# Kernel tuning notes

Measured on AMD Instinct MI355X. Metric: run time of the kernel, lower is better.

The kernel has to match this reference:

```python
import jax, jax.numpy as jnp
import numpy as np
import math

B, S, D, H = 2, 2048, 1024, 16
DH = D // H  # dim_per_head = 64


def setup_inputs() -> dict:
    key = jax.random.key(0)
    ks = jax.random.split(key, 12)
    s = 1.0 / math.sqrt(D)
    return {
        "key": jax.random.normal(ks[0], (B, S, D), jnp.float32),
        "value": jax.random.normal(ks[1], (B, S, D), jnp.float32),
        "query": jax.random.normal(ks[2], (B, S, D), jnp.float32),
        "mask": jax.random.randint(ks[3], (B, S, S), 0, 2).astype(bool),
        "Wq": jax.random.normal(ks[4], (D, D), jnp.float32) * s,
        "bq": jnp.zeros((D,), jnp.float32),
        "Wk": jax.random.normal(ks[5], (D, D), jnp.float32) * s,
        "bk": jnp.zeros((D,), jnp.float32),
        "Wv": jax.random.normal(ks[6], (D, D), jnp.float32) * s,
        "bv": jnp.zeros((D,), jnp.float32),
        "Wo": jax.random.normal(ks[7], (D, D), jnp.float32) * s,
        "bo": jnp.zeros((D,), jnp.float32),
    }


def _shape(x):
    # [B, S, D] -> [B, H, S, DH]
    return x.reshape(B, -1, H, DH).transpose(0, 2, 1, 3)


def reference(key, value, query, mask, Wq, bq, Wk, bk, Wv, bv, Wo, bo):
    q = _shape(query @ Wq.T + bq)  # [B,H,Sq,DH]
    k = _shape(key @ Wk.T + bk)    # [B,H,Sk,DH]
    v = _shape(value @ Wv.T + bv)  # [B,H,Sk,DH]
    q = q / jnp.sqrt(jnp.asarray(DH, q.dtype))
    scores = jnp.einsum("bhqd,bhkd->bhqk", q, k)
    scores = jnp.where(mask[:, None, :, :], jnp.asarray(-1e18, scores.dtype), scores)
    attn = jax.nn.softmax(scores, axis=-1)
    # dropout is identity in eval/deterministic reference
    ctx = jnp.einsum("bhqk,bhkd->bhqd", attn, v)
    ctx = ctx.transpose(0, 2, 1, 3).reshape(B, -1, D)  # unshape
    return ctx @ Wo.T + bo
```

## Files before the change

### kernel.cpp

```cpp
#include <hip/hip_runtime.h>
#include <math.h>


constexpr int Bc  = 2;
constexpr int Sc  = 2048;
constexpr int Dc  = 1024;
constexpr int Hc  = 16;
constexpr int DHc = 64;
constexpr int BSc = Bc * Sc;

constexpr float LOG2E = 1.4426950408889634f;

typedef __bf16 bf16x8 __attribute__((ext_vector_type(8)));
typedef __bf16 bf16x4 __attribute__((ext_vector_type(4)));
typedef __bf16 bf16x2 __attribute__((ext_vector_type(2)));
typedef float  f32x4  __attribute__((ext_vector_type(4)));
typedef float  f32x16 __attribute__((ext_vector_type(16)));
typedef unsigned uint32x2 __attribute__((ext_vector_type(2)));
typedef unsigned uint32x4 __attribute__((ext_vector_type(4)));

#define GLDS16(gp, lp) __builtin_amdgcn_global_load_lds( \
    (const __attribute__((address_space(1))) void*)(gp), \
    (__attribute__((address_space(3))) void*)(lp), 16, 0, 0)

__global__ __launch_bounds__(256)
void wsplit(const float* __restrict__ W0, const float* __restrict__ W1,
            const float* __restrict__ W2, const float* __restrict__ W3,
            __bf16* __restrict__ out)
{
    const float* src[4] = {W0, W1, W2, W3};
    const int z = blockIdx.y;
    const size_t idx = ((size_t)blockIdx.x * 256 + threadIdx.x) * 4;
    const float4 v = *(const float4*)&src[z][idx];
    bf16x4 o;
    o[0] = (__bf16)v.x; o[1] = (__bf16)v.y; o[2] = (__bf16)v.z; o[3] = (__bf16)v.w;
    *(bf16x4*)&out[(size_t)z * Dc * Dc + idx] = o;
}

__global__ __launch_bounds__(256)
void acast(const float* __restrict__ A0, const float* __restrict__ A1,
           const float* __restrict__ A2, __bf16* __restrict__ out)
{
    const float* src[3] = {A0, A1, A2};
    const int z = blockIdx.y;
    const size_t idx = ((size_t)blockIdx.x * 256 + threadIdx.x) * 8;
    const float4 a = *(const float4*)&src[z][idx];
    const float4 b = *(const float4*)&src[z][idx + 4];
    bf16x8 o;
    o[0] = (__bf16)a.x; o[1] = (__bf16)a.y; o[2] = (__bf16)a.z; o[3] = (__bf16)a.w;
    o[4] = (__bf16)b.x; o[5] = (__bf16)b.y; o[6] = (__bf16)b.z; o[7] = (__bf16)b.w;
    *(bf16x8*)&out[(size_t)z * BSc * Dc + idx] = o;
}

template<int KD>
__device__ __forceinline__ void sweep128bb(const __bf16* __restrict__ A,
                                           const __bf16* __restrict__ Wh,
                                           char* AsB, char* WsB,
                                           int gm0, int gn0, f32x4 acc[4][4])
{
    const int tid  = threadIdx.x;
    const int w    = tid >> 6;
    const int lane = tid & 63;
    const int cc   = lane & 15;
    const int g    = lane >> 4;
    const int wm   = (w & 1) * 64;
    const int wn   = (w >> 1) * 64;

    int wrow[4], wchk[4];
#pragma unroll
    for (int r = 0; r < 4; ++r) {
        const int L = r * 256 + tid;
        wrow[r] = L >> 3;
        wchk[r] = (L & 7) ^ (wrow[r] & 7);
    }

#pragma unroll
    for (int r = 0; r < 4; ++r) {
        GLDS16(Wh + (size_t)(gn0 + wrow[r]) * KD + wchk[r] * 8,
               WsB + (r * 256 + tid) * 16);
        GLDS16(A + (size_t)(gm0 + wrow[r]) * KD + wchk[r] * 8,
               AsB + (r * 256 + tid) * 16);
    }

    for (int it = 0; it < KD / 64; ++it) {
        const char* As = AsB + (it & 1) * 16384;
        const char* Ws = WsB + (it & 1) * 16384;
        __syncthreads();

        if (it + 1 < KD / 64) {
            const int kn = (it + 1) * 64;
            char* Wn = WsB + ((it + 1) & 1) * 16384;
            char* An = AsB + ((it + 1) & 1) * 16384;
#pragma unroll
            for (int r = 0; r < 4; ++r) {
                GLDS16(Wh + (size_t)(gn0 + wrow[r]) * KD + kn + wchk[r] * 8,
                       Wn + (r * 256 + tid) * 16);
                GLDS16(A + (size_t)(gm0 + wrow[r]) * KD + kn + wchk[r] * 8,
                       An + (r * 256 + tid) * 16);
            }
        }

        __builtin_amdgcn_s_setprio(1);
#pragma unroll
        for (int kk = 0; kk < 2; ++kk) {
            const int cb4 = (kk * 4 + g) << 4;
            bf16x8 af[4], bfr[4];
#pragma unroll
            for (int mt = 0; mt < 4; ++mt) {
                const int row = wm + mt * 16 + cc;
                af[mt] = *(const bf16x8*)(As + row * 128 + (cb4 ^ ((row & 7) << 4)));
            }
#pragma unroll
            for (int nt = 0; nt < 4; ++nt) {
                const int row = wn + nt * 16 + cc;
                bfr[nt] = *(const bf16x8*)(Ws + row * 128 + (cb4 ^ ((row & 7) << 4)));
            }
#pragma unroll
            for (int mt = 0; mt < 4; ++mt)
#pragma unroll
                for (int nt = 0; nt < 4; ++nt)
                    acc[mt][nt] = __builtin_amdgcn_mfma_f32_16x16x32_bf16(
                        af[mt], bfr[nt], acc[mt][nt], 0, 0, 0);
        }
        __builtin_amdgcn_s_setprio(0);
    }
}

__device__ __forceinline__ void sweep64p(const __bf16* __restrict__ Ahi,
                                         const __bf16* __restrict__ Alo,
                                         const __bf16* __restrict__ Wh,
                                         char* WsB, char* AhB, char* AlB,
                                         int gm0, int gn0, f32x4 acc[2][4])
{
    const int tid  = threadIdx.x;
    const int w    = tid >> 6;
    const int lane = tid & 63;
    const int cc   = lane & 15;
    const int g    = lane >> 4;
    const int wm   = (w & 1) * 32;
    const int wn   = (w >> 1) * 64;

    int wrow[4], wchk[4];
#pragma unroll
    for (int r = 0; r < 4; ++r) {
        const int L = r * 256 + tid;
        wrow[r] = L >> 3;
        wchk[r] = (L & 7) ^ (wrow[r] & 7);
    }
    int arow[2], achk[2];
#pragma unroll
    for (int r = 0; r < 2; ++r) {
        const int L = r * 256 + tid;
        arow[r] = L >> 3;
        achk[r] = (L & 7) ^ (arow[r] & 7);
    }

#pragma unroll
    for (int r = 0; r < 4; ++r)
        GLDS16(Wh + (size_t)(gn0 + wrow[r]) * Dc + wchk[r] * 8,
               WsB + (r * 256 + tid) * 16);
#pragma unroll
    for (int r = 0; r < 2; ++r) {
        GLDS16(Ahi + (size_t)(gm0 + arow[r]) * Dc + achk[r] * 8,
               AhB + (r * 256 + tid) * 16);
        GLDS16(Alo + (size_t)(gm0 + arow[r]) * Dc + achk[r] * 8,
               AlB + (r * 256 + tid) * 16);
    }

    for (int it = 0; it < Dc / 64; ++it) {
        const char* Ws = WsB + (it & 1) * 16384;
        const char* Ah = AhB + (it & 1) * 8192;
        const char* Al = AlB + (it & 1) * 8192;
        __syncthreads();

        if (it + 1 < Dc / 64) {
            const int kn = (it + 1) * 64;
            char* Wn = WsB + ((it + 1) & 1) * 16384;
            char* Hn = AhB + ((it + 1) & 1) * 8192;
            char* Ln = AlB + ((it + 1) & 1) * 8192;
#pragma unroll
            for (int r = 0; r < 4; ++r)
                GLDS16(Wh + (size_t)(gn0 + wrow[r]) * Dc + kn + wchk[r] * 8,
                       Wn + (r * 256 + tid) * 16);
#pragma unroll
            for (int r = 0; r < 2; ++r) {
                GLDS16(Ahi + (size_t)(gm0 + arow[r]) * Dc + kn + achk[r] * 8,
                       Hn + (r * 256 + tid) * 16);
                GLDS16(Alo + (size_t)(gm0 + arow[r]) * Dc + kn + achk[r] * 8,
                       Ln + (r * 256 + tid) * 16);
            }
        }

        __builtin_amdgcn_s_setprio(1);
#pragma unroll
        for (int kk = 0; kk < 2; ++kk) {
            const int cb4 = (kk * 4 + g) << 4;
            bf16x8 ahi[2], alo[2], bfr[4];
#pragma unroll
            for (int mt = 0; mt < 2; ++mt) {
                const int row = wm + mt * 16 + cc;
                const int off = row * 128 + (cb4 ^ ((row & 7) << 4));
                ahi[mt] = *(const bf16x8*)(Ah + off);
                alo[mt] = *(const bf16x8*)(Al + off);
            }
#pragma unroll
            for (int nt = 0; nt < 4; ++nt) {
                const int row = wn + nt * 16 + cc;
                bfr[nt] = *(const bf16x8*)(Ws + row * 128 + (cb4 ^ ((row & 7) << 4)));
            }
#pragma unroll
            for (int mt = 0; mt < 2; ++mt)
#pragma unroll
                for (int nt = 0; nt < 4; ++nt) {
                    acc[mt][nt] = __builtin_amdgcn_mfma_f32_16x16x32_bf16(
                        ahi[mt], bfr[nt], acc[mt][nt], 0, 0, 0);
                    acc[mt][nt] = __builtin_amdgcn_mfma_f32_16x16x32_bf16(
                        alo[mt], bfr[nt], acc[mt][nt], 0, 0, 0);
                }
        }
        __builtin_amdgcn_s_setprio(0);
    }
}

__global__ __launch_bounds__(256)
void qkv_mfma(const __bf16* __restrict__ Abf, const __bf16* __restrict__ Whi,
              const float* __restrict__ bq, const float* __restrict__ bk,
              const float* __restrict__ bv,
              __bf16* __restrict__ Qo, __bf16* __restrict__ Ko, __bf16* __restrict__ Vt)
{
    __shared__ __align__(16) char smem[65536];

    const int z = blockIdx.y;
    const float* bias = (z == 0) ? bq : (z == 1) ? bk : bv;
    const float scale = (z == 0) ? 0.125f * LOG2E : 1.0f;
    const __bf16* A   = Abf + (size_t)z * BSc * Dc;
    const __bf16* Wh  = Whi + (size_t)z * Dc * Dc;

    const int lb  = (blockIdx.x & 7) * 32 + (blockIdx.x >> 3);
    const int idx = lb & 31;
    const int gm0 = ((lb >> 5) * 4 + (idx & 3)) * 128;
    const int gn0 = (idx >> 2) * 128;

    f32x4 acc[4][4];
#pragma unroll
    for (int mt = 0; mt < 4; ++mt)
#pragma unroll
        for (int nt = 0; nt < 4; ++nt) acc[mt][nt] = {0.f, 0.f, 0.f, 0.f};

    sweep128bb<Dc>(A, Wh, smem, smem + 32768, gm0, gn0, acc);

    const int tid = threadIdx.x;
    const int w = tid >> 6, lane = tid & 63;
    const int cc = lane & 15, g = lane >> 4;
    const int wm = (w & 1) * 64, wn = (w >> 1) * 64;

    float bias4[4];
#pragma unroll
    for (int nt = 0; nt < 4; ++nt) bias4[nt] = bias[gn0 + wn + nt * 16 + cc];

    if (z == 2) {
#pragma unroll
        for (int mt = 0; mt < 4; ++mt)
#pragma unroll
            for (int nt = 0; nt < 4; ++nt) {
                const int col = gn0 + wn + nt * 16 + cc;
                const int h = col >> 6, dh = col & 63;
                const int row0 = gm0 + wm + mt * 16 + g * 4;
                const int b = row0 >> 11, s0 = row0 & 2047;
                bf16x4 vv;
#pragma unroll
                for (int reg = 0; reg < 4; ++reg)
                    vv[reg] = (__bf16)(acc[mt][nt][reg] + bias4[nt]);
                *(bf16x4*)&Vt[(((size_t)(b * Hc + h)) * DHc + dh) * Sc + s0] = vv;
            }
    } else {
        __bf16* O = (z == 0) ? Qo : Ko;
#pragma unroll
        for (int mt = 0; mt < 4; ++mt)
#pragma unroll
            for (int nt = 0; nt < 4; ++nt) {
                const int col = gn0 + wn + nt * 16 + cc;
                const int h = col >> 6, dh = col & 63;
#pragma unroll
                for (int reg = 0; reg < 4; ++reg) {
                    const int row = gm0 + wm + mt * 16 + g * 4 + reg;
                    const int b = row >> 11, s = row & 2047;
                    O[(((size_t)(b * Hc + h)) * Sc + s) * DHc + dh] =
                        (__bf16)((acc[mt][nt][reg] + bias4[nt]) * scale);
                }
            }
    }
}

__global__ __launch_bounds__(256)
void out_mfma(const __bf16* __restrict__ ctxHi, const __bf16* __restrict__ ctxLo,
              const __bf16* __restrict__ Wohi,
              const float* __restrict__ bo, float* __restrict__ out)
{
    __shared__ __align__(16) char smem[65536];

    const int lb = (blockIdx.x & 7) * 64 + (blockIdx.x >> 3);
    const int gm0 = ((lb >> 6) * 8 + (lb & 7)) * 64;
    const int gn0 = ((lb >> 3) & 7) * 128;

    f32x4 acc[2][4];
#pragma unroll
    for (int mt = 0; mt < 2; ++mt)
#pragma unroll
        for (int nt = 0; nt < 4; ++nt) acc[mt][nt] = {0.f, 0.f, 0.f, 0.f};

    sweep64p(ctxHi, ctxLo, Wohi, smem, smem + 32768, smem + 49152, gm0, gn0, acc);

    const int tid = threadIdx.x;
    const int w = tid >> 6, lane = tid & 63;
    const int cc = lane & 15, g = lane >> 4;
    const int wm = (w & 1) * 32, wn = (w >> 1) * 64;

    float bias4[4];
#pragma unroll
    for (int nt = 0; nt < 4; ++nt) bias4[nt] = bo[gn0 + wn + nt * 16 + cc];

#pragma unroll
    for (int mt = 0; mt < 2; ++mt)
#pragma unroll
        for (int nt = 0; nt < 4; ++nt) {
            const int col = gn0 + wn + nt * 16 + cc;
#pragma unroll
            for (int reg = 0; reg < 4; ++reg) {
                const int row = gm0 + wm + mt * 16 + g * 4 + reg;
                out[(size_t)row * Dc + col] = acc[mt][nt][reg] + bias4[nt];
            }
        }
}

__global__ __launch_bounds__(256)
void mask_pack(const int* __restrict__ mask, unsigned long long* __restrict__ out)
{
    const int lane = threadIdx.x & 63;
    const size_t waveBase = ((size_t)blockIdx.x * 4 + (threadIdx.x >> 6)) * 256;
    unsigned long long b0 = __ballot(mask[waveBase + lane]        != 0);
    unsigned long long b1 = __ballot(mask[waveBase + 64 + lane]   != 0);
    unsigned long long b2 = __ballot(mask[waveBase + 128 + lane]  != 0);
    unsigned long long b3 = __ballot(mask[waveBase + 192 + lane]  != 0);
    if (lane == 0) {
        unsigned long long* dst = out + (waveBase >> 6);
        dst[0] = b0; dst[1] = b1; dst[2] = b2; dst[3] = b3;
    }
}

__global__ __launch_bounds__(256, 2)
void attn_mfma(const __bf16* __restrict__ Q, const __bf16* __restrict__ K,
               const __bf16* __restrict__ Vt,
               const unsigned long long* __restrict__ mp,
               __bf16* __restrict__ ctxHi, __bf16* __restrict__ ctxLo)
{
    __shared__ __align__(16) char smem[32768];

    const int tid  = threadIdx.x;
    const int w    = tid >> 6;
    const int lane = tid & 63;
    const int c    = lane & 31;
    const int u    = lane >> 5;
    const int bh   = blockIdx.y;
    const int b    = bh >> 4;
    const int h    = bh & 15;
    const int qw   = blockIdx.x * 128 + w * 32;

    const __bf16* Qb  = Q  + (size_t)bh * Sc * DHc;
    const __bf16* Kb  = K  + (size_t)bh * Sc * DHc;
    const __bf16* Vtb = Vt + (size_t)bh * DHc * Sc;

    bf16x8 qa[4];
#pragma unroll
    for (int ch = 0; ch < 4; ++ch)
        qa[ch] = *(const bf16x8*)&Qb[(size_t)(qw + c) * DHc + ch * 16 + u * 8];

    f32x16 o[2];
#pragma unroll
    for (int dt = 0; dt < 2; ++dt)
#pragma unroll
        for (int i = 0; i < 16; ++i) o[dt][i] = 0.f;
    float lp[4] = {0.f, 0.f, 0.f, 0.f};

    const int ci[2] = {tid, 256 + tid};
    int rowi[2], ski[2];
#pragma unroll
    for (int i = 0; i < 2; ++i) {
        rowi[i] = ci[i] >> 3;
        ski[i]  = (ci[i] & 7) ^ (rowi[i] & 7);
    }

#pragma unroll
    for (int i = 0; i < 2; ++i) {
        GLDS16(Kb + (size_t)rowi[i] * DHc + ski[i] * 8,
               smem + ci[i] * 16);
        GLDS16(Vtb + (size_t)rowi[i] * Sc + ski[i] * 8,
               smem + 8192 + ci[i] * 16);
    }

    for (int it = 0; it < 32; ++it) {
        const char* Ks = smem + (it & 1) * 16384;
        const char* Vs = Ks + 8192;

        __syncthreads();

        if (it + 1 < 32) {
            char* Kn = smem + ((it + 1) & 1) * 16384;
            const int kn = (it + 1) * 64;
#pragma unroll
            for (int i = 0; i < 2; ++i) {
                GLDS16(Kb + (size_t)(kn + rowi[i]) * DHc + ski[i] * 8,
                       Kn + ci[i] * 16);
                GLDS16(Vtb + (size_t)rowi[i] * Sc + kn + ski[i] * 8,
                       Kn + 8192 + ci[i] * 16);
            }
        }

        const unsigned long long mw =
            mp[((size_t)(b * Sc + qw + c) << 5) + it];

        f32x16 sc[2];
        __builtin_amdgcn_s_setprio(1);
#pragma unroll
        for (int nt = 0; nt < 2; ++nt) {
            f32x16 z;
#pragma unroll
            for (int i = 0; i < 16; ++i) z[i] = -24.f;
#pragma unroll
            for (int ch = 0; ch < 4; ++ch) {
                const int row = nt * 32 + c;
                const bf16x8 kb = *(const bf16x8*)
                    (Ks + row * 128 + ((ch * 32 + u * 16) ^ ((row & 7) << 4)));
                z = __builtin_amdgcn_mfma_f32_32x32x16_bf16(kb, qa[ch], z, 0, 0, 0);
            }
            sc[nt] = z;
        }
        __builtin_amdgcn_s_setprio(0);

        unsigned pk[2][4][2];
#pragma unroll
        for (int nt = 0; nt < 2; ++nt)
#pragma unroll
            for (int rr = 0; rr < 4; ++rr) {
                const unsigned nib =
                    (unsigned)(mw >> (nt * 32 + rr * 8 + u * 4)) & 0xFu;
                float pv[4];
#pragma unroll
                for (int r = 0; r < 4; ++r) {
                    float p = __builtin_amdgcn_exp2f(sc[nt][rr * 4 + r]);
                    p = (nib & (1u << r)) ? 0.f : p;
                    lp[rr] += p;
                    pv[r] = p;
                }
                bf16x2 t0; t0[0] = (__bf16)pv[0]; t0[1] = (__bf16)pv[1];
                bf16x2 t1; t1[0] = (__bf16)pv[2]; t1[1] = (__bf16)pv[3];
                pk[nt][rr][0] = __builtin_bit_cast(unsigned, t0);
                pk[nt][rr][1] = __builtin_bit_cast(unsigned, t1);
            }

        bf16x8 pa[4];
#pragma unroll
        for (int kc = 0; kc < 4; ++kc) {
            const int nt = kc >> 1;
            const int r0 = (kc & 1) * 2;
            uint32x2 s0 = __builtin_amdgcn_permlane32_swap(
                pk[nt][r0][0], pk[nt][r0 + 1][0], false, false);
            uint32x2 s1 = __builtin_amdgcn_permlane32_swap(
                pk[nt][r0][1], pk[nt][r0 + 1][1], false, false);
            uint32x4 wds;
            wds[0] = s0[0]; wds[1] = s1[0]; wds[2] = s0[1]; wds[3] = s1[1];
            pa[kc] = __builtin_bit_cast(bf16x8, wds);
        }

        __builtin_amdgcn_s_setprio(1);
#pragma unroll
        for (int dt = 0; dt < 2; ++dt)
#pragma unroll
            for (int kc = 0; kc < 4; ++kc) {
                const int row = dt * 32 + c;
                const bf16x8 vb = *(const bf16x8*)
                    (Vs + row * 128 + ((kc * 32 + u * 16) ^ ((row & 7) << 4)));
                o[dt] = __builtin_amdgcn_mfma_f32_32x32x16_bf16(pa[kc], vb, o[dt], 0, 0, 0);
            }
        __builtin_amdgcn_s_setprio(0);
    }

    float lsum = (lp[0] + lp[1]) + (lp[2] + lp[3]);
    lsum += __shfl_xor(lsum, 32);
    const float linv = 1.0f / lsum;

    float inv[16];
#pragma unroll
    for (int i = 0; i < 16; ++i)
        inv[i] = __shfl(linv, (i & 3) + 8 * (i >> 2) + 4 * u);

#pragma unroll
    for (int dt = 0; dt < 2; ++dt)
#pragma unroll
        for (int i = 0; i < 16; ++i) {
            const int q = qw + (i & 3) + 8 * (i >> 2) + 4 * u;
            const size_t idx = ((size_t)b * Sc + q) * Dc + h * 64 + dt * 32 + c;
            const float v = o[dt][i] * inv[i];
            const __bf16 hi = (__bf16)v;
            ctxHi[idx] = hi;
            ctxLo[idx] = (__bf16)(v - (float)hi);
        }
}

extern "C" void kernel_launch(void* const* d_in, const int* in_sizes, int n_in,
                              void* d_out, int out_size, void* d_ws, size_t ws_size,
                              hipStream_t stream)
{
    const float* key   = (const float*)d_in[0];
    const float* value = (const float*)d_in[1];
    const float* query = (const float*)d_in[2];
    const int*   mask  = (const int*)  d_in[3];
    const float* Wq    = (const float*)d_in[4];
    const float* bq    = (const float*)d_in[5];
    const float* Wk    = (const float*)d_in[6];
    const float* bk    = (const float*)d_in[7];
    const float* Wv    = (const float*)d_in[8];
    const float* bv    = (const float*)d_in[9];
    const float* Wo    = (const float*)d_in[10];
    const float* bo    = (const float*)d_in[11];
    float* out = (float*)d_out;

    char* wsb = (char*)d_ws;
    __bf16* Qbf  = (__bf16*)(wsb);
    __bf16* Kbf  = (__bf16*)(wsb + ((size_t)8  << 20));
    __bf16* Vt   = (__bf16*)(wsb + ((size_t)16 << 20));
    unsigned long long* mpk = (unsigned long long*)(wsb + ((size_t)32 << 20));
    __bf16* Whi  = (__bf16*)(wsb + ((size_t)33 << 20));
    __bf16* ctxHi = (__bf16*)(wsb + ((size_t)41 << 20));
    __bf16* ctxLo = (__bf16*)(wsb + ((size_t)49 << 20));
    __bf16* Abf  = (__bf16*)(wsb + ((size_t)57 << 20));

    dim3 gws(Dc * Dc / (256 * 4), 4);
    wsplit<<<gws, 256, 0, stream>>>(Wq, Wk, Wv, Wo, Whi);

    dim3 gac(BSc * Dc / (256 * 8), 3);
    acast<<<gac, 256, 0, stream>>>(query, key, value, Abf);

    dim3 gqkv(256, 3);
    qkv_mfma<<<gqkv, 256, 0, stream>>>(Abf, Whi, bq, bk, bv, Qbf, Kbf, Vt);

    const int mask_n = Bc * Sc * Sc;
    mask_pack<<<mask_n / 1024, 256, 0, stream>>>(mask, mpk);

    dim3 gattn(Sc / 128, Bc * Hc);
    attn_mfma<<<gattn, 256, 0, stream>>>(Qbf, Kbf, Vt, mpk, ctxHi, ctxLo);

    out_mfma<<<dim3(512), 256, 0, stream>>>(ctxHi, ctxLo, Whi + (size_t)3 * Dc * Dc,
                                            bo, out);
}
```

Measured before the change: 250.3 us.

## Fuse prep kernels into one launch and stage two KV tiles per barrier

```diff
diff --git a/kernel.cpp b/kernel.cpp
--- a/kernel.cpp
+++ b/kernel.cpp
@@ -24,32 +24,51 @@
     (__attribute__((address_space(3))) void*)(lp), 16, 0, 0)
 
 __global__ __launch_bounds__(256)
-void wsplit(const float* __restrict__ W0, const float* __restrict__ W1,
-            const float* __restrict__ W2, const float* __restrict__ W3,
-            __bf16* __restrict__ out)
-{
-    const float* src[4] = {W0, W1, W2, W3};
-    const int z = blockIdx.y;
-    const size_t idx = ((size_t)blockIdx.x * 256 + threadIdx.x) * 4;
-    const float4 v = *(const float4*)&src[z][idx];
-    bf16x4 o;
-    o[0] = (__bf16)v.x; o[1] = (__bf16)v.y; o[2] = (__bf16)v.z; o[3] = (__bf16)v.w;
-    *(bf16x4*)&out[(size_t)z * Dc * Dc + idx] = o;
-}
-
-__global__ __launch_bounds__(256)
-void acast(const float* __restrict__ A0, const float* __restrict__ A1,
-           const float* __restrict__ A2, __bf16* __restrict__ out)
-{
-    const float* src[3] = {A0, A1, A2};
-    const int z = blockIdx.y;
-    const size_t idx = ((size_t)blockIdx.x * 256 + threadIdx.x) * 8;
-    const float4 a = *(const float4*)&src[z][idx];
-    const float4 b = *(const float4*)&src[z][idx + 4];
-    bf16x8 o;
-    o[0] = (__bf16)a.x; o[1] = (__bf16)a.y; o[2] = (__bf16)a.z; o[3] = (__bf16)a.w;
-    o[4] = (__bf16)b.x; o[5] = (__bf16)b.y; o[6] = (__bf16)b.z; o[7] = (__bf16)b.w;
-    *(bf16x8*)&out[(size_t)z * BSc * Dc + idx] = o;
+void prep(const float* __restrict__ W0, const float* __restrict__ W1,
+          const float* __restrict__ W2, const float* __restrict__ W3,
+          __bf16* __restrict__ Whi,
+          const float* __restrict__ A0, const float* __restrict__ A1,
+          const float* __restrict__ A2, __bf16* __restrict__ Abf,
+          const int* __restrict__ mask, unsigned long long* __restrict__ mpk)
+{
+    const int bid = blockIdx.x;
+    const int tid = threadIdx.x;
+
+    if (bid < 4096) {
+        const float* src[4] = {W0, W1, W2, W3};
+        const int z  = bid >> 10;
+        const int bx = bid & 1023;
+        const size_t idx = ((size_t)bx * 256 + tid) * 4;
+        const float4 v = *(const float4*)&src[z][idx];
+        bf16x4 o;
+        o[0] = (__bf16)v.x; o[1] = (__bf16)v.y;
+        o[2] = (__bf16)v.z; o[3] = (__bf16)v.w;
+        *(bf16x4*)&Whi[(size_t)z * Dc * Dc + idx] = o;
+    } else if (bid < 10240) {
+        const float* src[3] = {A0, A1, A2};
+        const int lin = bid - 4096;
+        const int z  = lin >> 11;
+        const int bx = lin & 2047;
+        const size_t idx = ((size_t)bx * 256 + tid) * 8;
+        const float4 a = *(const float4*)&src[z][idx];
+        const float4 b = *(const float4*)&src[z][idx + 4];
+        bf16x8 o;
+        o[0] = (__bf16)a.x; o[1] = (__bf16)a.y; o[2] = (__bf16)a.z; o[3] = (__bf16)a.w;
+        o[4] = (__bf16)b.x; o[5] = (__bf16)b.y; o[6] = (__bf16)b.z; o[7] = (__bf16)b.w;
+        *(bf16x8*)&Abf[(size_t)z * BSc * Dc + idx] = o;
+    } else {
+        const int bx   = bid - 10240;
+        const int lane = tid & 63;
+        const size_t waveBase = ((size_t)bx * 4 + (tid >> 6)) * 256;
+        unsigned long long b0 = __ballot(mask[waveBase + lane]        != 0);
+        unsigned long long b1 = __ballot(mask[waveBase + 64 + lane]   != 0);
+        unsigned long long b2 = __ballot(mask[waveBase + 128 + lane]  != 0);
+        unsigned long long b3 = __ballot(mask[waveBase + 192 + lane]  != 0);
+        if (lane == 0) {
+            unsigned long long* dst = mpk + (waveBase >> 6);
+            dst[0] = b0; dst[1] = b1; dst[2] = b2; dst[3] = b3;
+        }
+    }
 }
 
 template<int KD>
@@ -333,19 +352,93 @@
         }
 }
 
-__global__ __launch_bounds__(256)
-void mask_pack(const int* __restrict__ mask, unsigned long long* __restrict__ out)
-{
-    const int lane = threadIdx.x & 63;
-    const size_t waveBase = ((size_t)blockIdx.x * 4 + (threadIdx.x >> 6)) * 256;
-    unsigned long long b0 = __ballot(mask[waveBase + lane]        != 0);
-    unsigned long long b1 = __ballot(mask[waveBase + 64 + lane]   != 0);
-    unsigned long long b2 = __ballot(mask[waveBase + 128 + lane]  != 0);
-    unsigned long long b3 = __ballot(mask[waveBase + 192 + lane]  != 0);
-    if (lane == 0) {
-        unsigned long long* dst = out + (waveBase >> 6);
-        dst[0] = b0; dst[1] = b1; dst[2] = b2; dst[3] = b3;
-    }
+__device__ __forceinline__ void stage_pair(const __bf16* Kb, const __bf16* Vtb,
+                                           char* H, int t0,
+                                           int rowi0, int ski0, int ci0,
+                                           int rowi1, int ski1, int ci1)
+{
+#pragma unroll
+    for (int s = 0; s < 2; ++s) {
+        char* B = H + s * 16384;
+        const int kn = (t0 + s) * 64;
+        GLDS16(Kb + (size_t)(kn + rowi0) * DHc + ski0 * 8, B + ci0 * 16);
+        GLDS16(Vtb + (size_t)rowi0 * Sc + kn + ski0 * 8, B + 8192 + ci0 * 16);
+        GLDS16(Kb + (size_t)(kn + rowi1) * DHc + ski1 * 8, B + ci1 * 16);
+        GLDS16(Vtb + (size_t)rowi1 * Sc + kn + ski1 * 8, B + 8192 + ci1 * 16);
+    }
+}
+
+__device__ __forceinline__ void tile_step(const char* Ks, const char* Vs,
+                                          const bf16x8 qa[4], const f32x16& zb,
+                                          unsigned long long mw, int c, int u,
+                                          float lp[4], f32x16 o[2])
+{
+    f32x16 sc[2];
+    __builtin_amdgcn_s_setprio(1);
+#pragma unroll
+    for (int nt = 0; nt < 2; ++nt) {
+        const int row = nt * 32 + c;
+        const int rx  = (row & 7) << 4;
+        const bf16x8 kb0 = *(const bf16x8*)(Ks + row * 128 + ((u * 16) ^ rx));
+        f32x16 z = __builtin_amdgcn_mfma_f32_32x32x16_bf16(kb0, qa[0], zb, 0, 0, 0);
+#pragma unroll
+        for (int ch = 1; ch < 4; ++ch) {
+            const bf16x8 kb = *(const bf16x8*)
+                (Ks + row * 128 + ((ch * 32 + u * 16) ^ rx));
+            z = __builtin_amdgcn_mfma_f32_32x32x16_bf16(kb, qa[ch], z, 0, 0, 0);
+        }
+        sc[nt] = z;
+    }
+    __builtin_amdgcn_s_setprio(0);
+
+    unsigned pk[2][4][2];
+#pragma unroll
+    for (int nt = 0; nt < 2; ++nt)
+#pragma unroll
+        for (int rr = 0; rr < 4; ++rr) {
+            const unsigned nib =
+                (unsigned)(mw >> (nt * 32 + rr * 8 + u * 4)) & 0xFu;
+            float pv[4];
+#pragma unroll
+            for (int r = 0; r < 4; ++r) {
+                float p = __builtin_amdgcn_exp2f(sc[nt][rr * 4 + r]);
+                p = (nib & (1u << r)) ? 0.f : p;
+                lp[rr] += p;
+                pv[r] = p;
+            }
+            bf16x2 t0; t0[0] = (__bf16)pv[0]; t0[1] = (__bf16)pv[1];
+            bf16x2 t1; t1[0] = (__bf16)pv[2]; t1[1] = (__bf16)pv[3];
+            pk[nt][rr][0] = __builtin_bit_cast(unsigned, t0);
+            pk[nt][rr][1] = __builtin_bit_cast(unsigned, t1);
+        }
+
+    bf16x8 pa[4];
+#pragma unroll
+    for (int kc = 0; kc < 4; ++kc) {
+        const int nt = kc >> 1;
+        const int r0 = (kc & 1) * 2;
+        uint32x2 w0 = __builtin_amdgcn_permlane32_swap(
+            pk[nt][r0][0], pk[nt][r0 + 1][0], false, false);
+        uint32x2 w1 = __builtin_amdgcn_permlane32_swap(
+            pk[nt][r0][1], pk[nt][r0 + 1][1], false, false);
+        uint32x4 wds;
+        wds[0] = w0[0]; wds[1] = w1[0]; wds[2] = w0[1]; wds[3] = w1[1];
+        pa[kc] = __builtin_bit_cast(bf16x8, wds);
+    }
+
+    __builtin_amdgcn_s_setprio(1);
+#pragma unroll
+    for (int dt = 0; dt < 2; ++dt) {
+        const int row = dt * 32 + c;
+        const int rx  = (row & 7) << 4;
+#pragma unroll
+        for (int kc = 0; kc < 4; ++kc) {
+            const bf16x8 vb = *(const bf16x8*)
+                (Vs + row * 128 + ((kc * 32 + u * 16) ^ rx));
+            o[dt] = __builtin_amdgcn_mfma_f32_32x32x16_bf16(pa[kc], vb, o[dt], 0, 0, 0);
+        }
+    }
+    __builtin_amdgcn_s_setprio(0);
 }
 
 __global__ __launch_bounds__(256, 2)
@@ -354,7 +447,7 @@
                const unsigned long long* __restrict__ mp,
                __bf16* __restrict__ ctxHi, __bf16* __restrict__ ctxLo)
 {
-    __shared__ __align__(16) char smem[32768];
+    __shared__ __align__(16) char smem[65536];
 
     const int tid  = threadIdx.x;
     const int w    = tid >> 6;
@@ -375,114 +468,32 @@
     for (int ch = 0; ch < 4; ++ch)
         qa[ch] = *(const bf16x8*)&Qb[(size_t)(qw + c) * DHc + ch * 16 + u * 8];
 
-    f32x16 o[2];
-#pragma unroll
-    for (int dt = 0; dt < 2; ++dt)
-#pragma unroll
-        for (int i = 0; i < 16; ++i) o[dt][i] = 0.f;
+    f32x16 o[2], zb;
+#pragma unroll
+    for (int i = 0; i < 16; ++i) { o[0][i] = 0.f; o[1][i] = 0.f; zb[i] = -24.f; }
     float lp[4] = {0.f, 0.f, 0.f, 0.f};
 
-    const int ci[2] = {tid, 256 + tid};
-    int rowi[2], ski[2];
-#pragma unroll
-    for (int i = 0; i < 2; ++i) {
-        rowi[i] = ci[i] >> 3;
-        ski[i]  = (ci[i] & 7) ^ (rowi[i] & 7);
-    }
-
-#pragma unroll
-    for (int i = 0; i < 2; ++i) {
-        GLDS16(Kb + (size_t)rowi[i] * DHc + ski[i] * 8,
-               smem + ci[i] * 16);
-        GLDS16(Vtb + (size_t)rowi[i] * Sc + ski[i] * 8,
-               smem + 8192 + ci[i] * 16);
-    }
-
-    for (int it = 0; it < 32; ++it) {
-        const char* Ks = smem + (it & 1) * 16384;
-        const char* Vs = Ks + 8192;
-
+    const int ci0 = tid,        ci1 = 256 + tid;
+    const int rowi0 = ci0 >> 3, rowi1 = ci1 >> 3;
+    const int ski0 = (ci0 & 7) ^ (rowi0 & 7);
+    const int ski1 = (ci1 & 7) ^ (rowi1 & 7);
+
+    const size_t mbase = ((size_t)(b * Sc + qw + c) << 5);
+
+    stage_pair(Kb, Vtb, smem, 0, rowi0, ski0, ci0, rowi1, ski1, ci1);
+
+    for (int j = 0; j < 16; ++j) {
         __syncthreads();
-
-        if (it + 1 < 32) {
-            char* Kn = smem + ((it + 1) & 1) * 16384;
-            const int kn = (it + 1) * 64;
-#pragma unroll
-            for (int i = 0; i < 2; ++i) {
-                GLDS16(Kb + (size_t)(kn + rowi[i]) * DHc + ski[i] * 8,
-                       Kn + ci[i] * 16);
-                GLDS16(Vtb + (size_t)rowi[i] * Sc + kn + ski[i] * 8,
-                       Kn + 8192 + ci[i] * 16);
-            }
-        }
-
-        const unsigned long long mw =
-            mp[((size_t)(b * Sc + qw + c) << 5) + it];
-
-        f32x16 sc[2];
-        __builtin_amdgcn_s_setprio(1);
-#pragma unroll
-        for (int nt = 0; nt < 2; ++nt) {
-            f32x16 z;
-#pragma unroll
-            for (int i = 0; i < 16; ++i) z[i] = -24.f;
-#pragma unroll
-            for (int ch = 0; ch < 4; ++ch) {
-                const int row = nt * 32 + c;
-                const bf16x8 kb = *(const bf16x8*)
-                    (Ks + row * 128 + ((ch * 32 + u * 16) ^ ((row & 7) << 4)));
-                z = __builtin_amdgcn_mfma_f32_32x32x16_bf16(kb, qa[ch], z, 0, 0, 0);
-            }
-            sc[nt] = z;
-        }
-        __builtin_amdgcn_s_setprio(0);
-
-        unsigned pk[2][4][2];
-#pragma unroll
-        for (int nt = 0; nt < 2; ++nt)
-#pragma unroll
-            for (int rr = 0; rr < 4; ++rr) {
-                const unsigned nib =
-                    (unsigned)(mw >> (nt * 32 + rr * 8 + u * 4)) & 0xFu;
-                float pv[4];
-#pragma unroll
-                for (int r = 0; r < 4; ++r) {
-                    float p = __builtin_amdgcn_exp2f(sc[nt][rr * 4 + r]);
-                    p = (nib & (1u << r)) ? 0.f : p;
-                    lp[rr] += p;
-                    pv[r] = p;
-                }
-                bf16x2 t0; t0[0] = (__bf16)pv[0]; t0[1] = (__bf16)pv[1];
-                bf16x2 t1; t1[0] = (__bf16)pv[2]; t1[1] = (__bf16)pv[3];
-                pk[nt][rr][0] = __builtin_bit_cast(unsigned, t0);
-                pk[nt][rr][1] = __builtin_bit_cast(unsigned, t1);
-            }
-
-        bf16x8 pa[4];
-#pragma unroll
-        for (int kc = 0; kc < 4; ++kc) {
-            const int nt = kc >> 1;
-            const int r0 = (kc & 1) * 2;
-            uint32x2 s0 = __builtin_amdgcn_permlane32_swap(
-                pk[nt][r0][0], pk[nt][r0 + 1][0], false, false);
-            uint32x2 s1 = __builtin_amdgcn_permlane32_swap(
-                pk[nt][r0][1], pk[nt][r0 + 1][1], false, false);
-            uint32x4 wds;
-            wds[0] = s0[0]; wds[1] = s1[0]; wds[2] = s0[1]; wds[3] = s1[1];
-            pa[kc] = __builtin_bit_cast(bf16x8, wds);
-        }
-
-        __builtin_amdgcn_s_setprio(1);
-#pragma unroll
-        for (int dt = 0; dt < 2; ++dt)
-#pragma unroll
-            for (int kc = 0; kc < 4; ++kc) {
-                const int row = dt * 32 + c;
-                const bf16x8 vb = *(const bf16x8*)
-                    (Vs + row * 128 + ((kc * 32 + u * 16) ^ ((row & 7) << 4)));
-                o[dt] = __builtin_amdgcn_mfma_f32_32x32x16_bf16(pa[kc], vb, o[dt], 0, 0, 0);
-            }
-        __builtin_amdgcn_s_setprio(0);
+        if (j + 1 < 16)
+            stage_pair(Kb, Vtb, smem + ((j + 1) & 1) * 32768, 2 * j + 2,
+                       rowi0, ski0, ci0, rowi1, ski1, ci1);
+
+        const char* H = smem + (j & 1) * 32768;
+        const unsigned long long mw0 = mp[mbase + 2 * j];
+        const unsigned long long mw1 = mp[mbase + 2 * j + 1];
+
+        tile_step(H,         H + 8192,  qa, zb, mw0, c, u, lp, o);
+        tile_step(H + 16384, H + 24576, qa, zb, mw1, c, u, lp, o);
     }
 
     float lsum = (lp[0] + lp[1]) + (lp[2] + lp[3]);
@@ -535,18 +546,13 @@
     __bf16* ctxLo = (__bf16*)(wsb + ((size_t)49 << 20));
     __bf16* Abf  = (__bf16*)(wsb + ((size_t)57 << 20));
 
-    dim3 gws(Dc * Dc / (256 * 4), 4);
-    wsplit<<<gws, 256, 0, stream>>>(Wq, Wk, Wv, Wo, Whi);
-
-    dim3 gac(BSc * Dc / (256 * 8), 3);
-    acast<<<gac, 256, 0, stream>>>(query, key, value, Abf);
+    prep<<<dim3(18432), 256, 0, stream>>>(Wq, Wk, Wv, Wo, Whi,
+                                          query, key, value, Abf,
+                                          mask, mpk);
 
     dim3 gqkv(256, 3);
     qkv_mfma<<<gqkv, 256, 0, stream>>>(Abf, Whi, bq, bk, bv, Qbf, Kbf, Vt);
 
-    const int mask_n = Bc * Sc * Sc;
-    mask_pack<<<mask_n / 1024, 256, 0, stream>>>(mask, mpk);
-
     dim3 gattn(Sc / 128, Bc * Hc);
     attn_mfma<<<gattn, 256, 0, stream>>>(Qbf, Kbf, Vt, mpk, ctxHi, ctxLo);
 
```

New measurement: 247.9 us. No clear change (-1.0%).
